# Optimization experiments

Hardware: AMD Instinct MI355X
Metric: run time of the kernel (lower is better)

The kernel has to match this reference:

```python
import jax, jax.numpy as jnp
import numpy as np

N_HEADS = 4


def setup_inputs() -> dict:
    key = jax.random.key(0)
    ks = jax.random.split(key, 8)
    T, B, V, F = 30, 64, 32, 128   # len_pred, batch, n_vehicles, feature_size
    L, LF, TH = 64, 64, 20         # n_lanes, lane_feature_size, len_hist
    vehicles = jax.random.normal(ks[0], (T, B, V, F), dtype=jnp.float32)
    lanes = jax.random.normal(ks[1], (B, V, L, LF), dtype=jnp.float32)
    mask_lanes = jax.random.randint(ks[2], (TH, B, V, L), 0, 2).astype(bool)
    # torch Linear weight layout [out, in]; conv 1x1 weights squeezed to [out, in]
    Wk = jax.random.normal(ks[3], (F, LF), dtype=jnp.float32) / np.sqrt(LF)
    Wv = jax.random.normal(ks[4], (F, LF), dtype=jnp.float32) / np.sqrt(LF)
    Wq = jax.random.normal(ks[5], (F, F), dtype=jnp.float32) / np.sqrt(F)
    Wc = jax.random.normal(ks[6], (F, F), dtype=jnp.float32) / np.sqrt(F)
    return {"vehicles": vehicles, "lanes": lanes, "mask_lanes": mask_lanes,
            "Wk": Wk, "Wv": Wv, "Wq": Wq, "Wc": Wc}


def reference(vehicles, lanes, mask_lanes, Wk, Wv, Wq, Wc):
    # vehicles: [T,B,V,F], lanes: [B,V,L,LF], mask_lanes: [TH,B,V,L] bool
    T, B, V, F = vehicles.shape
    L = lanes.shape[2]
    H = N_HEADS
    hd = F // H
    # Linear projections of lanes (torch Linear: y = x @ W.T)
    k = jnp.einsum('bvlf,gf->bvlg', lanes, Wk).reshape(B, V, L, H, hd)
    v = jnp.einsum('bvlf,gf->bvlg', lanes, Wv).reshape(B, V, L, H, hd)
    # 1x1 Conv2d on feature channels == per-position linear
    q = jnp.einsum('tbvf,gf->tbvg', vehicles, Wq).reshape(T, B, V, H, hd)
    # mask: any over history dim -> [B,V,L] (the second any in attention is a no-op
    # since the mask is repeated identically over T and heads)
    mask = jnp.any(mask_lanes, axis=0)  # [B,V,L]
    scores = jnp.einsum('tbvhd,bvlhd->tbvhl', q, k) / jnp.sqrt(jnp.float32(hd))
    scores = jnp.where(mask[None, :, :, None, :], scores, jnp.float32(-1e9))
    p = jax.nn.softmax(scores, axis=-1)  # [T,B,V,H,L]
    out = jnp.einsum('tbvhl,bvlhd->tbvhd', p, v).reshape(T, B, V, F)
    out = jnp.einsum('tbvf,gf->tbvg', out, Wc) + vehicles
    return out
```

## Files before the change

### kernel.cpp

```cpp
#include <hip/hip_runtime.h>

#define T_  30
#define B_  64
#define V_  32
#define F_  128
#define L_  64
#define LF_ 64
#define TH_ 20
#define H_  4
#define HD_ 32

typedef __attribute__((ext_vector_type(8))) short bf16x8;
typedef __attribute__((ext_vector_type(4))) float f32x4;
#define MFMA(a,b,c) __builtin_amdgcn_mfma_f32_16x16x32_bf16(a, b, c, 0, 0, 0)

__device__ __forceinline__ float bf1(unsigned short u) {
    unsigned int x = ((unsigned int)u) << 16; float f; __builtin_memcpy(&f, &x, 4); return f;
}
__device__ __forceinline__ unsigned short f2bf(float f) {
    unsigned int x; __builtin_memcpy(&x, &f, 4);
    x += 0x7fffu + ((x >> 16) & 1u);
    return (unsigned short)(x >> 16);
}
__device__ __forceinline__ float4 ld4(const void* p, int idx4, bool isBf16) {
    if (isBf16) {
        ushort4 u = ((const ushort4*)p)[idx4];
        return make_float4(bf1(u.x), bf1(u.y), bf1(u.z), bf1(u.w));
    }
    return ((const float4*)p)[idx4];
}
__device__ __forceinline__ void st4bf(unsigned short* p, f32x4 v) {
    ushort4 u = { f2bf(v[0]), f2bf(v[1]), f2bf(v[2]), f2bf(v[3]) };
    *(ushort4*)p = u;
}
__device__ __forceinline__ bf16x8 ldWfrag(const void* W, int off, bool isBf16) {
    if (isBf16) return *(const bf16x8*)((const unsigned short*)W + off);
    const float* p = (const float*)W + off;
    float4 a = *(const float4*)p;
    float4 b = *(const float4*)(p + 4);
    bf16x8 r;
    r[0] = (short)f2bf(a.x); r[1] = (short)f2bf(a.y);
    r[2] = (short)f2bf(a.z); r[3] = (short)f2bf(a.w);
    r[4] = (short)f2bf(b.x); r[5] = (short)f2bf(b.y);
    r[6] = (short)f2bf(b.z); r[7] = (short)f2bf(b.w);
    return r;
}

__global__ __launch_bounds__(256, 2)
void lane_attn_kernel(const void* __restrict__ veh,
                      const void* __restrict__ lanes,
                      const void* __restrict__ maskp,
                      const void* __restrict__ Wk, const void* __restrict__ Wv,
                      const void* __restrict__ Wq, const void* __restrict__ Wc,
                      float* __restrict__ outp)
{
    const int bv   = blockIdx.x;
    const int tid  = threadIdx.x;
    const int w    = tid >> 6;
    const int lane = tid & 63;
    const int quad = lane >> 4;
    const int lm   = lane & 15;
    const int fbase = w * 32;

    __shared__ __align__(16) unsigned short sRegion[13824];
    __shared__ __align__(16) unsigned short sK [64 * 136];
    __shared__ __align__(16) unsigned short sVt[128 * 72];
    unsigned short* sQ     = sRegion;
    unsigned short* sO     = sRegion;
    unsigned short* sLanes = sRegion + 4352;
    unsigned short* sVehB  = sRegion + 9472;
    unsigned short* sS     = sRegion + 4352;

    const unsigned short* vh16 = (const unsigned short*)veh;
    const int field = (vh16[2 * lane] >> 7) & 0xFF;
    const bool isBf16 = __popcll(__ballot(field >= 100 && field <= 130)) >= 32;
    const unsigned char* mbp = (const unsigned char*)maskp;
    const bool maskByte = (__ballot(mbp[4 * lane + 1] != 0) != 0ULL);

    bool ok;
    {
        const int* mi = (const int*)maskp;
        int o = 0;
        #pragma unroll
        for (int th = 0; th < TH_; ++th) {
            const size_t e = (size_t)th * (B_ * V_ * L_) + (size_t)bv * L_ + lane;
            o |= maskByte ? (int)mbp[e] : mi[e];
        }
        ok = (o != 0);
    }

    bf16x8 wbK[2][2], wbV[2][2], wq[4][2];
    #pragma unroll
    for (int kt = 0; kt < 2; ++kt)
        #pragma unroll
        for (int nt = 0; nt < 2; ++nt) {
            const int off = (fbase + nt * 16 + lm) * 64 + kt * 32 + quad * 8;
            wbK[kt][nt] = ldWfrag(Wk, off, isBf16);
            wbV[kt][nt] = ldWfrag(Wv, off, isBf16);
        }
    #pragma unroll
    for (int kt = 0; kt < 4; ++kt)
        #pragma unroll
        for (int nt = 0; nt < 2; ++nt)
            wq[kt][nt] = ldWfrag(Wq, (fbase + nt * 16 + lm) * 128 + kt * 32 + quad * 8, isBf16);

    for (int u = tid; u < 64 * 16; u += 256) {
        const int l = u >> 4, c4 = u & 15;
        float4 x = ld4(lanes, bv * (L_ * LF_ / 4) + u, isBf16);
        ushort4 y = { f2bf(x.x), f2bf(x.y), f2bf(x.z), f2bf(x.w) };
        *(ushort4*)&sLanes[l * 80 + c4 * 4] = y;
    }
    for (int u = tid; u < 32 * 32; u += 256) {
        const int t = u >> 5, c4 = u & 31;
        ushort4 y = {0, 0, 0, 0};
        if (t < T_) {
            float4 x = ld4(veh, (t * (B_ * V_) + bv) * (F_ / 4) + c4, isBf16);
            y.x = f2bf(x.x); y.y = f2bf(x.y); y.z = f2bf(x.z); y.w = f2bf(x.w);
        }
        *(ushort4*)&sVehB[t * 136 + c4 * 4] = y;
    }
    __syncthreads();

    {
        f32x4 accK[2][4], accV[2][4];
        #pragma unroll
        for (int nt = 0; nt < 2; ++nt)
            #pragma unroll
            for (int mt = 0; mt < 4; ++mt) { accK[nt][mt] = (f32x4)0.f; accV[nt][mt] = (f32x4)0.f; }
        #pragma unroll
        for (int kt = 0; kt < 2; ++kt) {
            bf16x8 a[4];
            #pragma unroll
            for (int mt = 0; mt < 4; ++mt)
                a[mt] = *(const bf16x8*)&sLanes[(mt * 16 + lm) * 80 + kt * 32 + quad * 8];
            #pragma unroll
            for (int nt = 0; nt < 2; ++nt)
                #pragma unroll
                for (int mt = 0; mt < 4; ++mt) {
                    accK[nt][mt] = MFMA(a[mt], wbK[kt][nt], accK[nt][mt]);
                    accV[nt][mt] = MFMA(a[mt], wbV[kt][nt], accV[nt][mt]);
                }
        }
        #pragma unroll
        for (int nt = 0; nt < 2; ++nt) {
            const int f = fbase + nt * 16 + lm;
            #pragma unroll
            for (int mt = 0; mt < 4; ++mt) {
                const int l0 = mt * 16 + quad * 4;
                #pragma unroll
                for (int r = 0; r < 4; ++r) sK[(l0 + r) * 136 + f] = f2bf(accK[nt][mt][r]);
                st4bf(&sVt[f * 72 + l0], accV[nt][mt]);
            }
        }
    }

    {
        f32x4 acc[2][2];
        #pragma unroll
        for (int nt = 0; nt < 2; ++nt)
            #pragma unroll
            for (int mt = 0; mt < 2; ++mt) acc[nt][mt] = (f32x4)0.f;
        #pragma unroll
        for (int kt = 0; kt < 4; ++kt) {
            bf16x8 a[2];
            #pragma unroll
            for (int mt = 0; mt < 2; ++mt)
                a[mt] = *(const bf16x8*)&sVehB[(mt * 16 + lm) * 136 + kt * 32 + quad * 8];
            #pragma unroll
            for (int nt = 0; nt < 2; ++nt)
                #pragma unroll
                for (int mt = 0; mt < 2; ++mt) acc[nt][mt] = MFMA(a[mt], wq[kt][nt], acc[nt][mt]);
        }
        const float sc = 0.17677669529663687f;
        #pragma unroll
        for (int nt = 0; nt < 2; ++nt) {
            const int g = fbase + nt * 16 + lm;
            #pragma unroll
            for (int mt = 0; mt < 2; ++mt) {
                const int t0 = mt * 16 + quad * 4;
                #pragma unroll
                for (int r = 0; r < 4; ++r) sQ[(t0 + r) * 136 + g] = f2bf(acc[nt][mt][r] * sc);
            }
        }
    }

    bf16x8 wc[4][2];
    #pragma unroll
    for (int kt = 0; kt < 4; ++kt)
        #pragma unroll
        for (int nt = 0; nt < 2; ++nt)
            wc[kt][nt] = ldWfrag(Wc, (fbase + nt * 16 + lm) * 128 + kt * 32 + quad * 8, isBf16);

    __syncthreads();

    {
        bf16x8 a[4], b[2];
        #pragma unroll
        for (int mt = 0; mt < 4; ++mt)
            a[mt] = *(const bf16x8*)&sK[(mt * 16 + lm) * 136 + fbase + quad * 8];
        #pragma unroll
        for (int nt = 0; nt < 2; ++nt)
            b[nt] = *(const bf16x8*)&sQ[(nt * 16 + lm) * 136 + fbase + quad * 8];
        #pragma unroll
        for (int mt = 0; mt < 4; ++mt)
            #pragma unroll
            for (int nt = 0; nt < 2; ++nt) {
                f32x4 acc = MFMA(a[mt], b[nt], (f32x4)0.f);
                const int t = nt * 16 + lm;
                st4bf(&sS[(w * 32 + t) * 72 + mt * 16 + quad * 4], acc);
            }
    }

    {
        #pragma unroll
        for (int t = 0; t < T_; ++t) {
            const int idx = (w * 32 + t) * 72 + lane;
            const float p = ok ? __expf(bf1(sS[idx])) : 0.f;
            sS[idx] = f2bf(p);
        }
        sS[(w * 32 + 30) * 72 + lane] = 0;
        sS[(w * 32 + 31) * 72 + lane] = 0;
    }

    {
        bf16x8 bones;
        #pragma unroll
        for (int j = 0; j < 8; ++j) bones[j] = (short)0x3F80;
        f32x4 acc[2][2], ssum[2];
        #pragma unroll
        for (int mt = 0; mt < 2; ++mt) {
            ssum[mt] = (f32x4)0.f;
            #pragma unroll
            for (int nt = 0; nt < 2; ++nt) acc[mt][nt] = (f32x4)0.f;
        }
        #pragma unroll
        for (int kt = 0; kt < 2; ++kt) {
            bf16x8 a[2], b[2];
            #pragma unroll
            for (int mt = 0; mt < 2; ++mt)
                a[mt] = *(const bf16x8*)&sS[(w * 32 + mt * 16 + lm) * 72 + kt * 32 + quad * 8];
            #pragma unroll
            for (int nt = 0; nt < 2; ++nt)
                b[nt] = *(const bf16x8*)&sVt[(fbase + nt * 16 + lm) * 72 + kt * 32 + quad * 8];
            #pragma unroll
            for (int mt = 0; mt < 2; ++mt) {
                ssum[mt] = MFMA(a[mt], bones, ssum[mt]);
                #pragma unroll
                for (int nt = 0; nt < 2; ++nt) acc[mt][nt] = MFMA(a[mt], b[nt], acc[mt][nt]);
            }
        }
        #pragma unroll
        for (int mt = 0; mt < 2; ++mt)
            #pragma unroll
            for (int r = 0; r < 4; ++r) {
                const float s = ssum[mt][r];
                const float inv = (s > 0.f) ? 1.f / s : 0.f;
                const int t = mt * 16 + quad * 4 + r;
                #pragma unroll
                for (int nt = 0; nt < 2; ++nt)
                    sO[t * 136 + fbase + nt * 16 + lm] = f2bf(acc[mt][nt][r] * inv);
            }
    }

    float res[2][2][4];
    #pragma unroll
    for (int nt = 0; nt < 2; ++nt) {
        const int g = fbase + nt * 16 + lm;
        #pragma unroll
        for (int mt = 0; mt < 2; ++mt)
            #pragma unroll
            for (int r = 0; r < 4; ++r) {
                const int t = mt * 16 + quad * 4 + r;
                float v = 0.f;
                if (t < T_) {
                    const size_t off = ((size_t)t * (B_ * V_) + bv) * F_ + g;
                    v = isBf16 ? bf1(((const unsigned short*)veh)[off])
                               : ((const float*)veh)[off];
                }
                res[nt][mt][r] = v;
            }
    }
    __syncthreads();

    {
        f32x4 acc[2][2];
        #pragma unroll
        for (int nt = 0; nt < 2; ++nt)
            #pragma unroll
            for (int mt = 0; mt < 2; ++mt) acc[nt][mt] = (f32x4)0.f;
        #pragma unroll
        for (int kt = 0; kt < 4; ++kt) {
            bf16x8 a[2];
            #pragma unroll
            for (int mt = 0; mt < 2; ++mt)
                a[mt] = *(const bf16x8*)&sO[(mt * 16 + lm) * 136 + kt * 32 + quad * 8];
            #pragma unroll
            for (int nt = 0; nt < 2; ++nt)
                #pragma unroll
                for (int mt = 0; mt < 2; ++mt) acc[nt][mt] = MFMA(a[mt], wc[kt][nt], acc[nt][mt]);
        }
        #pragma unroll
        for (int nt = 0; nt < 2; ++nt) {
            const int g = fbase + nt * 16 + lm;
            #pragma unroll
            for (int mt = 0; mt < 2; ++mt)
                #pragma unroll
                for (int r = 0; r < 4; ++r) {
                    const int t = mt * 16 + quad * 4 + r;
                    if (t < T_) {
                        const size_t off = ((size_t)t * (B_ * V_) + bv) * F_ + g;
                        outp[off] = acc[nt][mt][r] + res[nt][mt][r];
                    }
                }
        }
    }
}

extern "C" void kernel_launch(void* const* d_in, const int* in_sizes, int n_in,
                              void* d_out, int out_size, void* d_ws, size_t ws_size,
                              hipStream_t stream) {
    (void)in_sizes; (void)n_in; (void)out_size; (void)d_ws; (void)ws_size;
    lane_attn_kernel<<<dim3(B_ * V_), dim3(256), 0, stream>>>(
        d_in[0], d_in[1], d_in[2], d_in[3], d_in[4], d_in[5], d_in[6],
        (float*)d_out);
}
```

Measured before the change: 190.6 us.

## Split each head across two waves and fuse softmax exp into score MFMA epilogue

Doubles the block to 512 threads so each head is handled by two waves, each owning half of the output feature columns or query rows. This halves per-thread register fragments and accumulators to raise occupancy and latency hiding. It also folds the masked exponentiation into the QK^T epilogue using a ballot-derived lane mask, removing the separate pass that read and rewrote the score buffer in shared memory. The cost is that per-wave work per barrier shrinks, so synchronisation overhead is relatively larger, and the mask and weight reads are duplicated across waves.

Measured after the change: 171.5 us. -10.1%, faster.

```diff
diff --git a/kernel.cpp b/kernel.cpp
--- a/kernel.cpp
+++ b/kernel.cpp
@@ -46,7 +46,7 @@
     return r;
 }
 
-__global__ __launch_bounds__(256, 2)
+__global__ __launch_bounds__(512, 4)
 void lane_attn_kernel(const void* __restrict__ veh,
                       const void* __restrict__ lanes,
                       const void* __restrict__ maskp,
@@ -54,13 +54,16 @@
                       const void* __restrict__ Wq, const void* __restrict__ Wc,
                       float* __restrict__ outp)
 {
-    const int bv   = blockIdx.x;
-    const int tid  = threadIdx.x;
-    const int w    = tid >> 6;
-    const int lane = tid & 63;
-    const int quad = lane >> 4;
-    const int lm   = lane & 15;
-    const int fbase = w * 32;
+    const int bv    = blockIdx.x;
+    const int tid   = threadIdx.x;
+    const int w     = tid >> 6;
+    const int h     = w >> 1;
+    const int shalf = w & 1;
+    const int lane  = tid & 63;
+    const int quad  = lane >> 4;
+    const int lm    = lane & 15;
+    const int fbase = h * 32;
+    const int fs    = fbase + shalf * 16;
 
     __shared__ __align__(16) unsigned short sRegion[13824];
     __shared__ __align__(16) unsigned short sK [64 * 136];
@@ -88,29 +91,26 @@
         }
         ok = (o != 0);
     }
-
-    bf16x8 wbK[2][2], wbV[2][2], wq[4][2];
+    const unsigned long long mok = __ballot(ok);
+
+    bf16x8 wbK[2], wbV[2], wq[4];
     #pragma unroll
-    for (int kt = 0; kt < 2; ++kt)
-        #pragma unroll
-        for (int nt = 0; nt < 2; ++nt) {
-            const int off = (fbase + nt * 16 + lm) * 64 + kt * 32 + quad * 8;
-            wbK[kt][nt] = ldWfrag(Wk, off, isBf16);
-            wbV[kt][nt] = ldWfrag(Wv, off, isBf16);
-        }
+    for (int kt = 0; kt < 2; ++kt) {
+        const int off = (fs + lm) * 64 + kt * 32 + quad * 8;
+        wbK[kt] = ldWfrag(Wk, off, isBf16);
+        wbV[kt] = ldWfrag(Wv, off, isBf16);
+    }
     #pragma unroll
     for (int kt = 0; kt < 4; ++kt)
-        #pragma unroll
-        for (int nt = 0; nt < 2; ++nt)
-            wq[kt][nt] = ldWfrag(Wq, (fbase + nt * 16 + lm) * 128 + kt * 32 + quad * 8, isBf16);
-
-    for (int u = tid; u < 64 * 16; u += 256) {
+        wq[kt] = ldWfrag(Wq, (fs + lm) * 128 + kt * 32 + quad * 8, isBf16);
+
+    for (int u = tid; u < 64 * 16; u += 512) {
         const int l = u >> 4, c4 = u & 15;
         float4 x = ld4(lanes, bv * (L_ * LF_ / 4) + u, isBf16);
         ushort4 y = { f2bf(x.x), f2bf(x.y), f2bf(x.z), f2bf(x.w) };
         *(ushort4*)&sLanes[l * 80 + c4 * 4] = y;
     }
-    for (int u = tid; u < 32 * 32; u += 256) {
+    for (int u = tid; u < 32 * 32; u += 512) {
         const int t = u >> 5, c4 = u & 31;
         ushort4 y = {0, 0, 0, 0};
         if (t < T_) {
@@ -122,11 +122,9 @@
     __syncthreads();
 
     {
-        f32x4 accK[2][4], accV[2][4];
-        #pragma unroll
-        for (int nt = 0; nt < 2; ++nt)
-            #pragma unroll
-            for (int mt = 0; mt < 4; ++mt) { accK[nt][mt] = (f32x4)0.f; accV[nt][mt] = (f32x4)0.f; }
+        f32x4 accK[4], accV[4];
+        #pragma unroll
+        for (int mt = 0; mt < 4; ++mt) { accK[mt] = (f32x4)0.f; accV[mt] = (f32x4)0.f; }
         #pragma unroll
         for (int kt = 0; kt < 2; ++kt) {
             bf16x8 a[4];
@@ -134,32 +132,24 @@
             for (int mt = 0; mt < 4; ++mt)
                 a[mt] = *(const bf16x8*)&sLanes[(mt * 16 + lm) * 80 + kt * 32 + quad * 8];
             #pragma unroll
-            for (int nt = 0; nt < 2; ++nt)
-                #pragma unroll
-                for (int mt = 0; mt < 4; ++mt) {
-                    accK[nt][mt] = MFMA(a[mt], wbK[kt][nt], accK[nt][mt]);
-                    accV[nt][mt] = MFMA(a[mt], wbV[kt][nt], accV[nt][mt]);
-                }
-        }
-        #pragma unroll
-        for (int nt = 0; nt < 2; ++nt) {
-            const int f = fbase + nt * 16 + lm;
-            #pragma unroll
             for (int mt = 0; mt < 4; ++mt) {
-                const int l0 = mt * 16 + quad * 4;
-                #pragma unroll
-                for (int r = 0; r < 4; ++r) sK[(l0 + r) * 136 + f] = f2bf(accK[nt][mt][r]);
-                st4bf(&sVt[f * 72 + l0], accV[nt][mt]);
+                accK[mt] = MFMA(a[mt], wbK[kt], accK[mt]);
+                accV[mt] = MFMA(a[mt], wbV[kt], accV[mt]);
             }
         }
-    }
-
-    {
-        f32x4 acc[2][2];
-        #pragma unroll
-        for (int nt = 0; nt < 2; ++nt)
-            #pragma unroll
-            for (int mt = 0; mt < 2; ++mt) acc[nt][mt] = (f32x4)0.f;
+        const int f = fs + lm;
+        #pragma unroll
+        for (int mt = 0; mt < 4; ++mt) {
+            const int l0 = mt * 16 + quad * 4;
+            #pragma unroll
+            for (int r = 0; r < 4; ++r) sK[(l0 + r) * 136 + f] = f2bf(accK[mt][r]);
+            st4bf(&sVt[f * 72 + l0], accV[mt]);
+        }
+    }
+
+    {
+        f32x4 acc[2];
+        acc[0] = (f32x4)0.f; acc[1] = (f32x4)0.f;
         #pragma unroll
         for (int kt = 0; kt < 4; ++kt) {
             bf16x8 a[2];
@@ -167,105 +157,77 @@
             for (int mt = 0; mt < 2; ++mt)
                 a[mt] = *(const bf16x8*)&sVehB[(mt * 16 + lm) * 136 + kt * 32 + quad * 8];
             #pragma unroll
-            for (int nt = 0; nt < 2; ++nt)
-                #pragma unroll
-                for (int mt = 0; mt < 2; ++mt) acc[nt][mt] = MFMA(a[mt], wq[kt][nt], acc[nt][mt]);
+            for (int mt = 0; mt < 2; ++mt) acc[mt] = MFMA(a[mt], wq[kt], acc[mt]);
         }
         const float sc = 0.17677669529663687f;
-        #pragma unroll
-        for (int nt = 0; nt < 2; ++nt) {
-            const int g = fbase + nt * 16 + lm;
-            #pragma unroll
-            for (int mt = 0; mt < 2; ++mt) {
-                const int t0 = mt * 16 + quad * 4;
-                #pragma unroll
-                for (int r = 0; r < 4; ++r) sQ[(t0 + r) * 136 + g] = f2bf(acc[nt][mt][r] * sc);
-            }
-        }
-    }
-
-    bf16x8 wc[4][2];
+        const int g = fs + lm;
+        #pragma unroll
+        for (int mt = 0; mt < 2; ++mt) {
+            const int t0 = mt * 16 + quad * 4;
+            #pragma unroll
+            for (int r = 0; r < 4; ++r) sQ[(t0 + r) * 136 + g] = f2bf(acc[mt][r] * sc);
+        }
+    }
+
+    bf16x8 wc[4];
     #pragma unroll
     for (int kt = 0; kt < 4; ++kt)
-        #pragma unroll
-        for (int nt = 0; nt < 2; ++nt)
-            wc[kt][nt] = ldWfrag(Wc, (fbase + nt * 16 + lm) * 128 + kt * 32 + quad * 8, isBf16);
+        wc[kt] = ldWfrag(Wc, (fs + lm) * 128 + kt * 32 + quad * 8, isBf16);
 
     __syncthreads();
 
     {
-        bf16x8 a[4], b[2];
+        bf16x8 a[4], b;
         #pragma unroll
         for (int mt = 0; mt < 4; ++mt)
             a[mt] = *(const bf16x8*)&sK[(mt * 16 + lm) * 136 + fbase + quad * 8];
-        #pragma unroll
-        for (int nt = 0; nt < 2; ++nt)
-            b[nt] = *(const bf16x8*)&sQ[(nt * 16 + lm) * 136 + fbase + quad * 8];
-        #pragma unroll
-        for (int mt = 0; mt < 4; ++mt)
-            #pragma unroll
-            for (int nt = 0; nt < 2; ++nt) {
-                f32x4 acc = MFMA(a[mt], b[nt], (f32x4)0.f);
-                const int t = nt * 16 + lm;
-                st4bf(&sS[(w * 32 + t) * 72 + mt * 16 + quad * 4], acc);
-            }
-    }
-
-    {
-        #pragma unroll
-        for (int t = 0; t < T_; ++t) {
-            const int idx = (w * 32 + t) * 72 + lane;
-            const float p = ok ? __expf(bf1(sS[idx])) : 0.f;
-            sS[idx] = f2bf(p);
-        }
-        sS[(w * 32 + 30) * 72 + lane] = 0;
-        sS[(w * 32 + 31) * 72 + lane] = 0;
+        b = *(const bf16x8*)&sQ[(shalf * 16 + lm) * 136 + fbase + quad * 8];
+        const int t = shalf * 16 + lm;
+        const bool tok = (t < T_);
+        #pragma unroll
+        for (int mt = 0; mt < 4; ++mt) {
+            f32x4 acc = MFMA(a[mt], b, (f32x4)0.f);
+            const int l0 = mt * 16 + quad * 4;
+            ushort4 y;
+            y.x = f2bf((tok && ((mok >> (l0 + 0)) & 1)) ? __expf(acc[0]) : 0.f);
+            y.y = f2bf((tok && ((mok >> (l0 + 1)) & 1)) ? __expf(acc[1]) : 0.f);
+            y.z = f2bf((tok && ((mok >> (l0 + 2)) & 1)) ? __expf(acc[2]) : 0.f);
+            y.w = f2bf((tok && ((mok >> (l0 + 3)) & 1)) ? __expf(acc[3]) : 0.f);
+            *(ushort4*)&sS[(h * 32 + t) * 72 + l0] = y;
+        }
     }
 
     {
         bf16x8 bones;
         #pragma unroll
         for (int j = 0; j < 8; ++j) bones[j] = (short)0x3F80;
-        f32x4 acc[2][2], ssum[2];
-        #pragma unroll
-        for (int mt = 0; mt < 2; ++mt) {
-            ssum[mt] = (f32x4)0.f;
-            #pragma unroll
-            for (int nt = 0; nt < 2; ++nt) acc[mt][nt] = (f32x4)0.f;
-        }
+        f32x4 acc[2], ssum;
+        acc[0] = (f32x4)0.f; acc[1] = (f32x4)0.f; ssum = (f32x4)0.f;
         #pragma unroll
         for (int kt = 0; kt < 2; ++kt) {
-            bf16x8 a[2], b[2];
-            #pragma unroll
-            for (int mt = 0; mt < 2; ++mt)
-                a[mt] = *(const bf16x8*)&sS[(w * 32 + mt * 16 + lm) * 72 + kt * 32 + quad * 8];
+            bf16x8 a = *(const bf16x8*)&sS[(h * 32 + shalf * 16 + lm) * 72 + kt * 32 + quad * 8];
+            bf16x8 b[2];
             #pragma unroll
             for (int nt = 0; nt < 2; ++nt)
                 b[nt] = *(const bf16x8*)&sVt[(fbase + nt * 16 + lm) * 72 + kt * 32 + quad * 8];
-            #pragma unroll
-            for (int mt = 0; mt < 2; ++mt) {
-                ssum[mt] = MFMA(a[mt], bones, ssum[mt]);
-                #pragma unroll
-                for (int nt = 0; nt < 2; ++nt) acc[mt][nt] = MFMA(a[mt], b[nt], acc[mt][nt]);
-            }
-        }
-        #pragma unroll
-        for (int mt = 0; mt < 2; ++mt)
-            #pragma unroll
-            for (int r = 0; r < 4; ++r) {
-                const float s = ssum[mt][r];
-                const float inv = (s > 0.f) ? 1.f / s : 0.f;
-                const int t = mt * 16 + quad * 4 + r;
-                #pragma unroll
-                for (int nt = 0; nt < 2; ++nt)
-                    sO[t * 136 + fbase + nt * 16 + lm] = f2bf(acc[mt][nt][r] * inv);
-            }
-    }
-
-    float res[2][2][4];
-    #pragma unroll
-    for (int nt = 0; nt < 2; ++nt) {
-        const int g = fbase + nt * 16 + lm;
+            ssum = MFMA(a, bones, ssum);
+            #pragma unroll
+            for (int nt = 0; nt < 2; ++nt) acc[nt] = MFMA(a, b[nt], acc[nt]);
+        }
+        #pragma unroll
+        for (int r = 0; r < 4; ++r) {
+            const float sv = ssum[r];
+            const float inv = (sv > 0.f) ? 1.f / sv : 0.f;
+            const int t = shalf * 16 + quad * 4 + r;
+            #pragma unroll
+            for (int nt = 0; nt < 2; ++nt)
+                sO[t * 136 + fbase + nt * 16 + lm] = f2bf(acc[nt][r] * inv);
+        }
+    }
+
+    float res[2][4];
+    {
+        const int g = fs + lm;
         #pragma unroll
         for (int mt = 0; mt < 2; ++mt)
             #pragma unroll
@@ -277,17 +239,14 @@
                     v = isBf16 ? bf1(((const unsigned short*)veh)[off])
                                : ((const float*)veh)[off];
                 }
-                res[nt][mt][r] = v;
+                res[mt][r] = v;
             }
     }
     __syncthreads();
 
     {
-        f32x4 acc[2][2];
-        #pragma unroll
-        for (int nt = 0; nt < 2; ++nt)
-            #pragma unroll
-            for (int mt = 0; mt < 2; ++mt) acc[nt][mt] = (f32x4)0.f;
+        f32x4 acc[2];
+        acc[0] = (f32x4)0.f; acc[1] = (f32x4)0.f;
         #pragma unroll
         for (int kt = 0; kt < 4; ++kt) {
             bf16x8 a[2];
@@ -295,24 +254,19 @@
             for (int mt = 0; mt < 2; ++mt)
                 a[mt] = *(const bf16x8*)&sO[(mt * 16 + lm) * 136 + kt * 32 + quad * 8];
             #pragma unroll
-            for (int nt = 0; nt < 2; ++nt)
-                #pragma unroll
-                for (int mt = 0; mt < 2; ++mt) acc[nt][mt] = MFMA(a[mt], wc[kt][nt], acc[nt][mt]);
-        }
-        #pragma unroll
-        for (int nt = 0; nt < 2; ++nt) {
-            const int g = fbase + nt * 16 + lm;
-            #pragma unroll
-            for (int mt = 0; mt < 2; ++mt)
-                #pragma unroll
-                for (int r = 0; r < 4; ++r) {
-                    const int t = mt * 16 + quad * 4 + r;
-                    if (t < T_) {
-                        const size_t off = ((size_t)t * (B_ * V_) + bv) * F_ + g;
-                        outp[off] = acc[nt][mt][r] + res[nt][mt][r];
-                    }
+            for (int mt = 0; mt < 2; ++mt) acc[mt] = MFMA(a[mt], wc[kt], acc[mt]);
+        }
+        const int g = fs + lm;
+        #pragma unroll
+        for (int mt = 0; mt < 2; ++mt)
+            #pragma unroll
+            for (int r = 0; r < 4; ++r) {
+                const int t = mt * 16 + quad * 4 + r;
+                if (t < T_) {
+                    const size_t off = ((size_t)t * (B_ * V_) + bv) * F_ + g;
+                    outp[off] = acc[mt][r] + res[mt][r];
                 }
-        }
+            }
     }
 }
 
@@ -320,7 +274,7 @@
                               void* d_out, int out_size, void* d_ws, size_t ws_size,
                               hipStream_t stream) {
     (void)in_sizes; (void)n_in; (void)out_size; (void)d_ws; (void)ws_size;
-    lane_attn_kernel<<<dim3(B_ * V_), dim3(256), 0, stream>>>(
+    lane_attn_kernel<<<dim3(B_ * V_), dim3(512), 0, stream>>>(
         d_in[0], d_in[1], d_in[2], d_in[3], d_in[4], d_in[5], d_in[6],
         (float*)d_out);
 }
```
